# Kernel optimization log

Measured on AMD Instinct MI355X. Metric: run time of the kernel, lower is better.

The kernel has to match this reference:

```python
import jax, jax.numpy as jnp
import numpy as np

HIDDEN = 2048
N_HEADS = 16
HEAD_DIM = HIDDEN // N_HEADS
INV_NORM = 1.0 / float(np.sqrt(HEAD_DIM))
BETA = 1.0


def setup_inputs() -> dict:
    key = jax.random.key(0)
    ks = jax.random.split(key, 12)
    B, S, H = 2, 2048, HIDDEN
    scale = 1.0 / float(np.sqrt(H))
    return {
        "hidden_states": jax.random.normal(ks[0], (B, S, H), jnp.float32),
        "residual": jax.random.normal(ks[1], (B, S, H), jnp.float32),
        "alibi": jax.random.normal(ks[2], (B * N_HEADS, 1, S), jnp.float32),
        "Wq": jax.random.normal(ks[3], (H, H), jnp.float32) * scale,
        "bq": jnp.zeros((H,), jnp.float32),
        "Wk": jax.random.normal(ks[4], (H, H), jnp.float32) * scale,
        "bk": jnp.zeros((H,), jnp.float32),
        "Wv": jax.random.normal(ks[5], (H, H), jnp.float32) * scale,
        "bv": jnp.zeros((H,), jnp.float32),
        "Wd": jax.random.normal(ks[6], (H, H), jnp.float32) * scale,
        "bd": jnp.zeros((H,), jnp.float32),
    }


def reference(hidden_states, residual, alibi, Wq, bq, Wk, bk, Wv, bv, Wd, bd):
    B, S, H = hidden_states.shape
    # separate QKV projections (nn.Linear: x @ W^T + b)
    q = hidden_states @ Wq.T + bq
    k = hidden_states @ Wk.T + bk
    v = hidden_states @ Wv.T + bv
    # [B, n_heads, S, head_dim]
    q = q.reshape(B, S, N_HEADS, HEAD_DIM).transpose(0, 2, 1, 3)
    k = k.reshape(B, S, N_HEADS, HEAD_DIM).transpose(0, 2, 1, 3)
    v = v.reshape(B, S, N_HEADS, HEAD_DIM).transpose(0, 2, 1, 3)
    # baddbmm: scores = beta * alibi + inv_norm * q @ k^T, per (batch*head)
    alibi_bh = alibi.reshape(B, N_HEADS, 1, S)  # broadcasts over query dim
    scores = BETA * alibi_bh + INV_NORM * jnp.einsum("bhqd,bhkd->bhqk", q, k)
    probs = jax.nn.softmax(scores.astype(jnp.float32), axis=-1).astype(v.dtype)
    # attention dropout: p=0.0 (identity)
    ctx = jnp.einsum("bhqk,bhkd->bhqd", probs, v)  # [B,H,S,D]
    ctx = ctx.transpose(0, 2, 1, 3).reshape(B, S, H)
    out = ctx @ Wd.T + bd
    # hidden dropout p=0.0 then residual add (dropout_add)
    return out + residual
```

## Files before the change

kernel.cpp:

```cpp
#include <hip/hip_runtime.h>

#define HID   2048
#define NHEAD 16
#define HD    128
#define SEQ   2048
#define BATCH 2
#define MROWS (BATCH*SEQ)
#define NQKV  (3*HID)
#define INV_NORM 0.08838834764831845f
#define LOG2E    1.4426950408889634f
#define SCALE_L2 (INV_NORM*LOG2E)

typedef __attribute__((ext_vector_type(8)))  __bf16 bf16x8;
typedef __attribute__((ext_vector_type(4)))  float  f32x4;
typedef __attribute__((ext_vector_type(16))) float  f32x16;

typedef __attribute__((address_space(1))) void GV;
typedef __attribute__((address_space(3))) void LV;

__device__ __forceinline__ void async16(const void* g, void* l) {
  __builtin_amdgcn_global_load_lds((const GV*)g, (LV*)l, 16, 0, 0);
}

__device__ __forceinline__ unsigned short f2bf(float f) {
  unsigned u = __builtin_bit_cast(unsigned, f);
  u += 0x7FFFu + ((u >> 16) & 1u);
  return (unsigned short)(u >> 16);
}

__device__ __forceinline__ unsigned pkbf(float a, float b) {
#if __has_builtin(__builtin_amdgcn_cvt_pk_bf16_f32)
  typedef __attribute__((ext_vector_type(2))) __bf16 bf16x2;
  bf16x2 r = __builtin_amdgcn_cvt_pk_bf16_f32(a, b);
  return __builtin_bit_cast(unsigned, r);
#else
  return (unsigned)f2bf(a) | ((unsigned)f2bf(b) << 16);
#endif
}

__device__ __forceinline__ void pl32swap(unsigned &a, unsigned &b) {
#if __has_builtin(__builtin_amdgcn_permlane32_swap)
  typedef __attribute__((ext_vector_type(2))) unsigned u32x2;
  u32x2 r = __builtin_amdgcn_permlane32_swap(a, b, false, false);
  a = r[0]; b = r[1];
#else
  asm volatile("v_permlane32_swap_b32 %0, %1" : "+v"(a), "+v"(b));
#endif
}

__device__ __forceinline__ void mfma16(f32x4& c, bf16x8 a, bf16x8 b) {
  c = __builtin_amdgcn_mfma_f32_16x16x32_bf16(a, b, c, 0, 0, 0);
}

__device__ __forceinline__ bf16x8 frag(const unsigned short* buf, int row, int chunk) {
  return *(const bf16x8*)(buf + ((row * 8 + (chunk ^ (row & 7))) << 3));
}

__global__ __launch_bounds__(256) void cvt_all_kernel(
    const float* __restrict__ hidden,
    const float* __restrict__ W0, const float* __restrict__ W1,
    const float* __restrict__ W2, const float* __restrict__ W3,
    unsigned short* __restrict__ Xb) {
  const int sel = blockIdx.y;
  const float* src;
  unsigned short* dst;
  int n;
  if (sel == 0) { src = hidden; dst = Xb; n = MROWS * HID; }
  else {
    src = (sel == 1) ? W0 : (sel == 2) ? W1 : (sel == 3) ? W2 : W3;
    dst = Xb + (size_t)MROWS * HID + (size_t)(sel - 1) * HID * HID;
    n = HID * HID;
  }
  int i = (blockIdx.x * 256 + threadIdx.x) * 4;
  if (i >= n) return;
  float4 v = *(const float4*)(src + i);
  ushort4 o;
  o.x = f2bf(v.x); o.y = f2bf(v.y); o.z = f2bf(v.z); o.w = f2bf(v.w);
  *(ushort4*)(dst + i) = o;
}

#define BUFU (24576)
#define BUF3 (3 * BUFU)

__global__ __launch_bounds__(512, 2) void gemm_qkv384_kernel(
    const unsigned short* __restrict__ Xb, const unsigned short* __restrict__ Wb,
    const float* __restrict__ bq, const float* __restrict__ bk,
    const float* __restrict__ bv, unsigned short* __restrict__ Cout) {
  __shared__ __align__(16) unsigned short smem[BUF3];

  const int tid  = threadIdx.x;
  const int w    = tid >> 6;
  const int lane = tid & 63;
  const int l16  = lane & 15;
  const int quad = lane >> 4;
  const int wm   = (w & 3) * 64;
  const int wn   = (w >> 2) * 64;

  const int wg = blockIdx.x;
  const int sw = (wg & 7) * 32 + (wg >> 3);
  const int m0  = (sw & 15) * 256;
  const int rn0 = (sw >> 4) * 384;

  const int sr  = tid >> 3;
  const int scs = ((tid & 7) ^ (sr & 7)) * 8;
  const unsigned short* aBase = Xb + (size_t)(m0 + sr) * HID + scs;

#define STGA(UB, RB, KT)                                              \
  async16(aBase + (size_t)(RB) * HID + (KT),                          \
          (char*)smem + (UB) * 2 + (RB) * 128 + w * 1024)
#define STGB(UB, RB, KT)                                              \
  async16(bBase + (size_t)(RB) * HID + (KT),                          \
          (char*)smem + (UB) * 2 + 32768 + (RB) * 128 + w * 1024)

#define VM6  asm volatile("s_waitcnt vmcnt(6)" ::: "memory")
#define VM0  asm volatile("s_waitcnt vmcnt(0)" ::: "memory")

#define PHASE(UB, KK, STGBLK, WAITBLK)                                         \
  {                                                                            \
    const unsigned short* Ab = smem + (UB);                                    \
    const unsigned short* Bb = Ab + 16384;                                     \
    bf16x8 ta[4], tb[4];                                                       \
    ta[0] = frag(Ab, wm + l16, (KK) * 4 + quad);                               \
    _Pragma("unroll")                                                          \
    for (int j = 0; j < 4; ++j)  tb[j] = frag(Bb, wn + j * 16 + l16, (KK) * 4 + quad); \
    _Pragma("unroll")                                                          \
    for (int ii = 1; ii < 4; ++ii) ta[ii] = frag(Ab, wm + ii * 16 + l16, (KK) * 4 + quad); \
    STGBLK;                                                                    \
    __builtin_amdgcn_s_setprio(1);                                             \
    _Pragma("unroll")                                                          \
    for (int ii = 0; ii < 4; ++ii)                                             \
      _Pragma("unroll")                                                        \
      for (int j = 0; j < 4; ++j) mfma16(acc[ii][j], ta[ii], tb[j]);           \
    __builtin_amdgcn_s_setprio(0);                                             \
    asm volatile("s_waitcnt lgkmcnt(0)" ::: "memory");                         \
    WAITBLK;                                                                   \
    __builtin_amdgcn_s_barrier();                                              \
  }

  for (int p = 0; p < 3; ++p) {
    const unsigned short* bBase = Wb + (size_t)(rn0 + p * 128 + sr) * HID + scs;

    f32x4 acc[4][4];
    const f32x4 zero = {0.f, 0.f, 0.f, 0.f};
#pragma unroll
    for (int a = 0; a < 4; ++a)
#pragma unroll
      for (int j = 0; j < 4; ++j) acc[a][j] = zero;

    STGA(0, 0, 0);  STGA(0, 64, 0);  STGA(0, 128, 0);  STGA(0, 192, 0);
    STGB(0, 0, 0);  STGB(0, 64, 0);
    STGA(BUFU, 0, 64);  STGA(BUFU, 64, 64);  STGA(BUFU, 128, 64);  STGA(BUFU, 192, 64);
    STGB(BUFU, 0, 64);  STGB(BUFU, 64, 64);
    VM6;
    __builtin_amdgcn_s_barrier();

    int kb = 0;
    for (int g = 0; g < 5; ++g) {
      PHASE(0,        0, { STGA(2*BUFU, 0, kb+128); STGA(2*BUFU, 64, kb+128); STGA(2*BUFU, 128, kb+128); }, {});
      PHASE(0,        1, { STGA(2*BUFU, 192, kb+128); STGB(2*BUFU, 0, kb+128); STGB(2*BUFU, 64, kb+128); }, VM6);
      PHASE(BUFU,     0, { STGA(0, 0, kb+192); STGA(0, 64, kb+192); STGA(0, 128, kb+192); }, {});
      PHASE(BUFU,     1, { STGA(0, 192, kb+192); STGB(0, 0, kb+192); STGB(0, 64, kb+192); }, VM6);
      PHASE(2*BUFU,   0, { STGA(BUFU, 0, kb+256); STGA(BUFU, 64, kb+256); STGA(BUFU, 128, kb+256); }, {});
      PHASE(2*BUFU,   1, { STGA(BUFU, 192, kb+256); STGB(BUFU, 0, kb+256); STGB(BUFU, 64, kb+256); }, VM6);
      PHASE(0,        0, { STGA(2*BUFU, 0, kb+320); STGA(2*BUFU, 64, kb+320); STGA(2*BUFU, 128, kb+320); }, {});
      PHASE(0,        1, { STGA(2*BUFU, 192, kb+320); STGB(2*BUFU, 0, kb+320); STGB(2*BUFU, 64, kb+320); }, VM6);
      PHASE(BUFU,     0, { STGA(0, 0, kb+384); STGA(0, 64, kb+384); STGA(0, 128, kb+384); }, {});
      PHASE(BUFU,     1, { STGA(0, 192, kb+384); STGB(0, 0, kb+384); STGB(0, 64, kb+384); }, VM6);
      PHASE(2*BUFU,   0, { STGA(BUFU, 0, kb+448); STGA(BUFU, 64, kb+448); STGA(BUFU, 128, kb+448); }, {});
      PHASE(2*BUFU,   1, { STGA(BUFU, 192, kb+448); STGB(BUFU, 0, kb+448); STGB(BUFU, 64, kb+448); }, VM6);
      kb += 384;
    }

    PHASE(0,    0, {}, {});
    PHASE(0,    1, {}, VM0);
    PHASE(BUFU, 0, {}, {});
    PHASE(BUFU, 1, {}, {});

#pragma unroll
    for (int j = 0; j < 4; ++j) {
      int ng = rn0 + p * 128 + wn + j * 16 + l16;
      float bias = (ng < HID) ? bq[ng] : (ng < 2 * HID ? bk[ng - HID] : bv[ng - 2 * HID]);
#pragma unroll
      for (int a = 0; a < 4; ++a)
#pragma unroll
        for (int r = 0; r < 4; ++r) {
          int mg = m0 + wm + a * 16 + quad * 4 + r;
          Cout[(size_t)mg * NQKV + ng] = f2bf(acc[a][j][r] + bias);
        }
    }
  }
#undef STGA
#undef STGB
#undef PHASE
#undef VM6
#undef VM0
}

__global__ __launch_bounds__(512, 2) void gemm_out384_kernel(
    const unsigned short* __restrict__ Ctx, const unsigned short* __restrict__ Wdb,
    const float* __restrict__ bd, const float* __restrict__ Res,
    float* __restrict__ Out) {
  __shared__ __align__(16) unsigned short smem[BUF3];

  const int tid  = threadIdx.x;
  const int w    = tid >> 6;
  const int lane = tid & 63;
  const int l16  = lane & 15;
  const int quad = lane >> 4;
  const int wm   = (w & 3) * 64;
  const int wn   = (w >> 2) * 64;

  const int wg = blockIdx.x;
  const int sw = (wg & 7) * 32 + (wg >> 3);
  const int m0  = (sw & 15) * 256;
  const int rn0 = (sw >> 4) * 128;

  const int sr  = tid >> 3;
  const int scs = ((tid & 7) ^ (sr & 7)) * 8;
  const unsigned short* aBase = Ctx + (size_t)(m0 + sr) * HID + scs;
  const unsigned short* bBase = Wdb + (size_t)(rn0 + sr) * HID + scs;

#define STGA(UB, RB, KT)                                              \
  async16(aBase + (size_t)(RB) * HID + (KT),                          \
          (char*)smem + (UB) * 2 + (RB) * 128 + w * 1024)
#define STGB(UB, RB, KT)                                              \
  async16(bBase + (size_t)(RB) * HID + (KT),                          \
          (char*)smem + (UB) * 2 + 32768 + (RB) * 128 + w * 1024)

#define VM6  asm volatile("s_waitcnt vmcnt(6)" ::: "memory")
#define VM0  asm volatile("s_waitcnt vmcnt(0)" ::: "memory")

#define PHASE(UB, KK, STGBLK, WAITBLK)                                         \
  {                                                                            \
    const unsigned short* Ab = smem + (UB);                                    \
    const unsigned short* Bb = Ab + 16384;                                     \
    bf16x8 ta[4], tb[4];                                                       \
    ta[0] = frag(Ab, wm + l16, (KK) * 4 + quad);                               \
    _Pragma("unroll")                                                          \
    for (int j = 0; j < 4; ++j)  tb[j] = frag(Bb, wn + j * 16 + l16, (KK) * 4 + quad); \
    _Pragma("unroll")                                                          \
    for (int ii = 1; ii < 4; ++ii) ta[ii] = frag(Ab, wm + ii * 16 + l16, (KK) * 4 + quad); \
    STGBLK;                                                                    \
    __builtin_amdgcn_s_setprio(1);                                             \
    _Pragma("unroll")                                                          \
    for (int ii = 0; ii < 4; ++ii)                                             \
      _Pragma("unroll")                                                        \
      for (int j = 0; j < 4; ++j) mfma16(acc[ii][j], ta[ii], tb[j]);           \
    __builtin_amdgcn_s_setprio(0);                                             \
    asm volatile("s_waitcnt lgkmcnt(0)" ::: "memory");                         \
    WAITBLK;                                                                   \
    __builtin_amdgcn_s_barrier();                                              \
  }

  f32x4 acc[4][4];
  const f32x4 zero = {0.f, 0.f, 0.f, 0.f};
#pragma unroll
  for (int a = 0; a < 4; ++a)
#pragma unroll
    for (int j = 0; j < 4; ++j) acc[a][j] = zero;

  STGA(0, 0, 0);  STGA(0, 64, 0);  STGA(0, 128, 0);  STGA(0, 192, 0);
  STGB(0, 0, 0);  STGB(0, 64, 0);
  STGA(BUFU, 0, 64);  STGA(BUFU, 64, 64);  STGA(BUFU, 128, 64);  STGA(BUFU, 192, 64);
  STGB(BUFU, 0, 64);  STGB(BUFU, 64, 64);
  VM6;
  __builtin_amdgcn_s_barrier();

  int kb = 0;
  for (int g = 0; g < 5; ++g) {
    PHASE(0,        0, { STGA(2*BUFU, 0, kb+128); STGA(2*BUFU, 64, kb+128); STGA(2*BUFU, 128, kb+128); }, {});
    PHASE(0,        1, { STGA(2*BUFU, 192, kb+128); STGB(2*BUFU, 0, kb+128); STGB(2*BUFU, 64, kb+128); }, VM6);
    PHASE(BUFU,     0, { STGA(0, 0, kb+192); STGA(0, 64, kb+192); STGA(0, 128, kb+192); }, {});
    PHASE(BUFU,     1, { STGA(0, 192, kb+192); STGB(0, 0, kb+192); STGB(0, 64, kb+192); }, VM6);
    PHASE(2*BUFU,   0, { STGA(BUFU, 0, kb+256); STGA(BUFU, 64, kb+256); STGA(BUFU, 128, kb+256); }, {});
    PHASE(2*BUFU,   1, { STGA(BUFU, 192, kb+256); STGB(BUFU, 0, kb+256); STGB(BUFU, 64, kb+256); }, VM6);
    PHASE(0,        0, { STGA(2*BUFU, 0, kb+320); STGA(2*BUFU, 64, kb+320); STGA(2*BUFU, 128, kb+320); }, {});
    PHASE(0,        1, { STGA(2*BUFU, 192, kb+320); STGB(2*BUFU, 0, kb+320); STGB(2*BUFU, 64, kb+320); }, VM6);
    PHASE(BUFU,     0, { STGA(0, 0, kb+384); STGA(0, 64, kb+384); STGA(0, 128, kb+384); }, {});
    PHASE(BUFU,     1, { STGA(0, 192, kb+384); STGB(0, 0, kb+384); STGB(0, 64, kb+384); }, VM6);
    PHASE(2*BUFU,   0, { STGA(BUFU, 0, kb+448); STGA(BUFU, 64, kb+448); STGA(BUFU, 128, kb+448); }, {});
    PHASE(2*BUFU,   1, { STGA(BUFU, 192, kb+448); STGB(BUFU, 0, kb+448); STGB(BUFU, 64, kb+448); }, VM6);
    kb += 384;
  }

  PHASE(0,    0, {}, {});
  PHASE(0,    1, {}, VM0);
  PHASE(BUFU, 0, {}, {});
  PHASE(BUFU, 1, {}, {});

#pragma unroll
  for (int j = 0; j < 4; ++j) {
    int ng = rn0 + wn + j * 16 + l16;
    float bias = bd[ng];
#pragma unroll
    for (int a = 0; a < 4; ++a)
#pragma unroll
      for (int r = 0; r < 4; ++r) {
        int mg = m0 + wm + a * 16 + quad * 4 + r;
        size_t off = (size_t)mg * HID + ng;
        Out[off] = acc[a][j][r] + bias + Res[off];
      }
  }
#undef STGA
#undef STGB
#undef PHASE
#undef VM6
#undef VM0
}

__global__ __launch_bounds__(256) void vtrans_kernel(const unsigned short* __restrict__ QKV,
                                                     unsigned short* __restrict__ Vt) {
  __shared__ __align__(16) unsigned short T[64][72];
  const int s0 = blockIdx.x * 64, d0 = blockIdx.y * 64, bh = blockIdx.z;
  const int b = bh >> 4, h = bh & 15;
  const int tid = threadIdx.x;
#pragma unroll
  for (int i = 0; i < 2; ++i) {
    int idx = i * 256 + tid;
    int r = idx >> 3, ch = idx & 7;
    const unsigned short* g = QKV + ((size_t)b * SEQ + s0 + r) * NQKV + 2 * HID + h * HD + d0 + ch * 8;
    *(uint4*)(&T[r][ch * 8]) = *(const uint4*)g;
  }
  __syncthreads();
#pragma unroll
  for (int i = 0; i < 2; ++i) {
    int idx = i * 256 + tid;
    int d = idx >> 3, ch = idx & 7;
    unsigned short v[8];
#pragma unroll
    for (int x = 0; x < 8; ++x) v[x] = T[ch * 8 + x][d];
    unsigned short* g = Vt + ((size_t)bh * HD + d0 + d) * SEQ + s0 + ch * 8;
    *(uint4*)g = *(const uint4*)v;
  }
}

__global__ __launch_bounds__(256, 2) void attn_kernel(
    const unsigned short* __restrict__ QKV, const unsigned short* __restrict__ Vt,
    const float* __restrict__ alibi, unsigned short* __restrict__ Ctx) {
  __shared__ __align__(16) char smem[73728];
  unsigned short* Ks0  = (unsigned short*)smem;
  unsigned short* Ks1  = (unsigned short*)(smem + 16384);
  unsigned short* Vts0 = (unsigned short*)(smem + 32768);
  unsigned short* Vts1 = (unsigned short*)(smem + 49152);
  float*          Alsf = (float*)(smem + 65536);
  unsigned short* Qs   = (unsigned short*)smem;

  const int tid = threadIdx.x, w = tid >> 6, lane = tid & 63;
  const int l32 = lane & 31, h = lane >> 5;
  const int bid = blockIdx.x;
  const int t  = bid >> 3;
  const int q0 = (t & 15) * 128;
  const int bh = (bid & 7) + 8 * (t >> 4);
  const int b = bh >> 4, hh = bh & 15;
  const size_t rowbase = (size_t)b * SEQ;
  const float* ali = alibi + (size_t)bh * SEQ;
  const unsigned short* Vbh = Vt + (size_t)bh * HD * SEQ;

  {
    const unsigned short* qbase = QKV + (rowbase + q0) * NQKV + hh * HD;
#pragma unroll
    for (int i = 0; i < 8; ++i) {
      int slot = i * 256 + w * 64 + lane;
      int r = slot >> 4, c = (slot & 15) ^ (r & 15);
      async16(qbase + (size_t)r * NQKV + c * 8, (char*)Qs + (size_t)(i * 256 + w * 64) * 16);
    }
    const char* asrc = (const char*)ali;
#pragma unroll
    for (int i = 0; i < 2; ++i) {
      int slot = i * 256 + w * 64 + lane;
      async16(asrc + (size_t)slot * 16, (char*)Alsf + (size_t)(i * 256 + w * 64) * 16);
    }
  }
  __syncthreads();
  bf16x8 qf[8];
  {
    int qr = w * 32 + l32;
#pragma unroll
    for (int ks = 0; ks < 8; ++ks) {
      int c = (ks * 2 + h) ^ (qr & 15);
      qf[ks] = *(const bf16x8*)(Qs + (qr * 16 + c) * 8);
    }
  }

  f32x16 oacc[4];
  float l_acc = 0.f;
#pragma unroll
  for (int nb = 0; nb < 4; ++nb)
#pragma unroll
    for (int r = 0; r < 16; ++r) oacc[nb][r] = 0.f;

  __syncthreads();

#define STAGE_KV(T, KD, VD)                                                      \
  {                                                                              \
    const unsigned short* kbase = QKV + (rowbase + (T) * 64) * NQKV + HID + hh * HD; \
    _Pragma("unroll")                                                            \
    for (int i = 0; i < 4; ++i) {                                                \
      int slot = i * 256 + w * 64 + lane;                                        \
      int r = slot >> 4, c = (slot & 15) ^ (r & 15);                             \
      async16(kbase + (size_t)r * NQKV + c * 8, (char*)(KD) + (size_t)(i * 256 + w * 64) * 16); \
    }                                                                            \
    const unsigned short* vbase = Vbh + (T) * 64;                                \
    _Pragma("unroll")                                                            \
    for (int i = 0; i < 4; ++i) {                                                \
      int slot = i * 256 + w * 64 + lane;                                        \
      int r = slot >> 3, c = (slot & 7) ^ (r & 7);                               \
      async16(vbase + (size_t)r * SEQ + c * 8, (char*)(VD) + (size_t)(i * 256 + w * 64) * 16); \
    }                                                                            \
  }

  STAGE_KV(0, Ks0, Vts0);
  STAGE_KV(1, Ks1, Vts1);
  asm volatile("s_waitcnt vmcnt(8)" ::: "memory");
  __builtin_amdgcn_s_barrier();

  for (int kt = 0; kt < SEQ / 64; ++kt) {
    const unsigned short* Kc = (kt & 1) ? Ks1 : Ks0;
    const unsigned short* Vc = (kt & 1) ? Vts1 : Vts0;

    f32x16 sacc[2];
#pragma unroll
    for (int mb = 0; mb < 2; ++mb)
#pragma unroll
      for (int r = 0; r < 16; ++r) sacc[mb][r] = 0.f;
    __builtin_amdgcn_s_setprio(1);
#pragma unroll
    for (int ks = 0; ks < 8; ++ks) {
#pragma unroll
      for (int mb = 0; mb < 2; ++mb) {
        bf16x8 kf = *(const bf16x8*)(Kc + ((mb * 32 + l32) * 16 + ((ks * 2 + h) ^ (l32 & 15))) * 8);
        sacc[mb] = __builtin_amdgcn_mfma_f32_32x32x16_bf16(kf, qf[ks], sacc[mb], 0, 0, 0);
      }
    }
    __builtin_amdgcn_s_setprio(0);

    const float* alsk = Alsf + kt * 64 + 4 * h;
    bf16x8 pfr[4];
#pragma unroll
    for (int mb = 0; mb < 2; ++mb) {
      float p[16];
#pragma unroll
      for (int g = 0; g < 4; ++g) {
        float4 av = *(const float4*)(alsk + mb * 32 + g * 8);
        p[g * 4 + 0] = __builtin_amdgcn_exp2f(sacc[mb][g * 4 + 0] * SCALE_L2 + av.x * LOG2E);
        p[g * 4 + 1] = __builtin_amdgcn_exp2f(sacc[mb][g * 4 + 1] * SCALE_L2 + av.y * LOG2E);
        p[g * 4 + 2] = __builtin_amdgcn_exp2f(sacc[mb][g * 4 + 2] * SCALE_L2 + av.z * LOG2E);
        p[g * 4 + 3] = __builtin_amdgcn_exp2f(sacc[mb][g * 4 + 3] * SCALE_L2 + av.w * LOG2E);
        l_acc += (p[g * 4 + 0] + p[g * 4 + 1]) + (p[g * 4 + 2] + p[g * 4 + 3]);
      }
      unsigned c0 = pkbf(p[0],  p[1]),  c1 = pkbf(p[2],  p[3]);
      unsigned c2 = pkbf(p[4],  p[5]),  c3 = pkbf(p[6],  p[7]);
      unsigned c4 = pkbf(p[8],  p[9]),  c5 = pkbf(p[10], p[11]);
      unsigned c6 = pkbf(p[12], p[13]), c7 = pkbf(p[14], p[15]);
      pl32swap(c0, c2);  pl32swap(c1, c3);
      pl32swap(c4, c6);  pl32swap(c5, c7);
      uint4 f0; f0.x = c0; f0.y = c1; f0.z = c2; f0.w = c3;
      uint4 f1; f1.x = c4; f1.y = c5; f1.z = c6; f1.w = c7;
      pfr[mb * 2 + 0] = __builtin_bit_cast(bf16x8, f0);
      pfr[mb * 2 + 1] = __builtin_bit_cast(bf16x8, f1);
    }

    __builtin_amdgcn_s_setprio(1);
#pragma unroll
    for (int ks2 = 0; ks2 < 4; ++ks2) {
      bf16x8 pf = pfr[ks2];
#pragma unroll
      for (int nb = 0; nb < 4; ++nb) {
        bf16x8 vf = *(const bf16x8*)(Vc + ((nb * 32 + l32) * 8 + ((ks2 * 2 + h) ^ (l32 & 7))) * 8);
        oacc[nb] = __builtin_amdgcn_mfma_f32_32x32x16_bf16(pf, vf, oacc[nb], 0, 0, 0);
      }
    }
    __builtin_amdgcn_s_setprio(0);

    asm volatile("s_waitcnt lgkmcnt(0) vmcnt(0)" ::: "memory");
    __builtin_amdgcn_s_barrier();
    if (kt + 2 < SEQ / 64) {
      unsigned short* kd = (kt & 1) ? Ks1 : Ks0;
      unsigned short* vd = (kt & 1) ? Vts1 : Vts0;
      STAGE_KV(kt + 2, kd, vd);
    }
  }
#undef STAGE_KV

  float lf = l_acc + __shfl_xor(l_acc, 32, 64);
  float rinv[16];
#pragma unroll
  for (int reg = 0; reg < 16; ++reg) {
    int row = (reg & 3) + 8 * (reg >> 2) + 4 * h;
    rinv[reg] = 1.0f / __shfl(lf, row, 64);
  }

#pragma unroll
  for (int nb = 0; nb < 4; ++nb)
#pragma unroll
    for (int reg = 0; reg < 16; ++reg) {
      int row = (reg & 3) + 8 * (reg >> 2) + 4 * h;
      size_t qg = rowbase + q0 + w * 32 + row;
      Ctx[qg * HID + hh * HD + nb * 32 + l32] = f2bf(oacc[nb][reg] * rinv[reg]);
    }
}

extern "C" void kernel_launch(void* const* d_in, const int* in_sizes, int n_in,
                              void* d_out, int out_size, void* d_ws, size_t ws_size,
                              hipStream_t stream) {
  const float* hidden   = (const float*)d_in[0];
  const float* residual = (const float*)d_in[1];
  const float* alibi    = (const float*)d_in[2];
  const float* Wq = (const float*)d_in[3];
  const float* bq = (const float*)d_in[4];
  const float* Wk = (const float*)d_in[5];
  const float* bk = (const float*)d_in[6];
  const float* Wv = (const float*)d_in[7];
  const float* bv = (const float*)d_in[8];
  const float* Wd = (const float*)d_in[9];
  const float* bd = (const float*)d_in[10];
  float* out = (float*)d_out;

  unsigned short* Xb    = (unsigned short*)d_ws;
  unsigned short* Wqkvb = Xb + (size_t)MROWS * HID;
  unsigned short* Wdb   = Wqkvb + (size_t)NQKV * HID;
  unsigned short* QKVb  = Wdb + (size_t)HID * HID;
  unsigned short* Ctxb  = QKVb + (size_t)MROWS * NQKV;
  unsigned short* Vtb   = Wqkvb;

  cvt_all_kernel<<<dim3(MROWS * HID / 4 / 256, 5), 256, 0, stream>>>(hidden, Wq, Wk, Wv, Wd, Xb);

  gemm_qkv384_kernel<<<256, 512, 0, stream>>>(Xb, Wqkvb, bq, bk, bv, QKVb);
  vtrans_kernel<<<dim3(SEQ / 64, HD / 64, BATCH * NHEAD), 256, 0, stream>>>(QKVb, Vtb);
  attn_kernel<<<512, 256, 0, stream>>>(QKVb, Vtb, alibi, Ctxb);
  gemm_out384_kernel<<<256, 512, 0, stream>>>(Ctxb, Wdb, bd, residual, out);
}
```

Baseline: 433.9 us.

## Software-pipeline attention QK^T with softmax/PV and flatten conversion grid

The attention loop is restructured into a two-tile software pipeline: the QK^T MFMAs for the next KV tile are issued alongside the softmax and PV of the current tile. K and V staging are split so each buffer is refilled as soon as it is consumed, with finer waitcnt/barrier placement. This is meant to hide exp/softmax latency behind matrix work and to overlap loads better, at the cost of more live accumulator registers and a hardcoded sequence-length schedule. The conversion kernel is also flattened to a 1D grid, which removes the idle blocks that the weight slices launched in the old 2D grid.

```diff
diff --git a/kernel.cpp b/kernel.cpp
--- a/kernel.cpp
+++ b/kernel.cpp
@@ -61,22 +61,20 @@
     const float* __restrict__ W0, const float* __restrict__ W1,
     const float* __restrict__ W2, const float* __restrict__ W3,
     unsigned short* __restrict__ Xb) {
-  const int sel = blockIdx.y;
+  size_t e = ((size_t)blockIdx.x * 256 + threadIdx.x) * 4;
   const float* src;
-  unsigned short* dst;
-  int n;
-  if (sel == 0) { src = hidden; dst = Xb; n = MROWS * HID; }
-  else {
-    src = (sel == 1) ? W0 : (sel == 2) ? W1 : (sel == 3) ? W2 : W3;
-    dst = Xb + (size_t)MROWS * HID + (size_t)(sel - 1) * HID * HID;
-    n = HID * HID;
-  }
-  int i = (blockIdx.x * 256 + threadIdx.x) * 4;
-  if (i >= n) return;
-  float4 v = *(const float4*)(src + i);
+  if (e < (size_t)MROWS * HID) {
+    src = hidden + e;
+  } else {
+    size_t r = e - (size_t)MROWS * HID;
+    int sel = (int)(r >> 22);
+    size_t off = r & ((1u << 22) - 1);
+    src = ((sel == 0) ? W0 : (sel == 1) ? W1 : (sel == 2) ? W2 : W3) + off;
+  }
+  float4 v = *(const float4*)src;
   ushort4 o;
   o.x = f2bf(v.x); o.y = f2bf(v.y); o.z = f2bf(v.z); o.w = f2bf(v.w);
-  *(ushort4*)(dst + i) = o;
+  *(ushort4*)(Xb + e) = o;
 }
 
 #define BUFU (24576)
@@ -391,15 +389,18 @@
 
   __syncthreads();
 
-#define STAGE_KV(T, KD, VD)                                                      \
+#define STAGE_K(T, KD)                                                           \
   {                                                                              \
-    const unsigned short* kbase = QKV + (rowbase + (T) * 64) * NQKV + HID + hh * HD; \
+    const unsigned short* kbase = QKV + (rowbase + (size_t)(T) * 64) * NQKV + HID + hh * HD; \
     _Pragma("unroll")                                                            \
     for (int i = 0; i < 4; ++i) {                                                \
       int slot = i * 256 + w * 64 + lane;                                        \
       int r = slot >> 4, c = (slot & 15) ^ (r & 15);                             \
       async16(kbase + (size_t)r * NQKV + c * 8, (char*)(KD) + (size_t)(i * 256 + w * 64) * 16); \
     }                                                                            \
+  }
+#define STAGE_V(T, VD)                                                           \
+  {                                                                              \
     const unsigned short* vbase = Vbh + (T) * 64;                                \
     _Pragma("unroll")                                                            \
     for (int i = 0; i < 4; ++i) {                                                \
@@ -409,78 +410,106 @@
     }                                                                            \
   }
 
-  STAGE_KV(0, Ks0, Vts0);
-  STAGE_KV(1, Ks1, Vts1);
+#define QKT(SACC, KBUF)                                                          \
+  {                                                                              \
+    _Pragma("unroll")                                                            \
+    for (int mb = 0; mb < 2; ++mb)                                               \
+      _Pragma("unroll")                                                          \
+      for (int r = 0; r < 16; ++r) (SACC)[mb][r] = 0.f;                          \
+    __builtin_amdgcn_s_setprio(1);                                               \
+    _Pragma("unroll")                                                            \
+    for (int ks = 0; ks < 8; ++ks)                                               \
+      _Pragma("unroll")                                                          \
+      for (int mb = 0; mb < 2; ++mb) {                                           \
+        bf16x8 kf = *(const bf16x8*)((KBUF) + ((mb * 32 + l32) * 16 + ((ks * 2 + h) ^ (l32 & 15))) * 8); \
+        (SACC)[mb] = __builtin_amdgcn_mfma_f32_32x32x16_bf16(kf, qf[ks], (SACC)[mb], 0, 0, 0); \
+      }                                                                          \
+    __builtin_amdgcn_s_setprio(0);                                               \
+  }
+
+#define SOFTMAX(SACC, KT, PFR)                                                   \
+  {                                                                              \
+    const float* alsk = Alsf + (KT) * 64 + 4 * h;                                \
+    _Pragma("unroll")                                                            \
+    for (int mb = 0; mb < 2; ++mb) {                                             \
+      float p[16];                                                               \
+      _Pragma("unroll")                                                          \
+      for (int g = 0; g < 4; ++g) {                                              \
+        float4 av = *(const float4*)(alsk + mb * 32 + g * 8);                    \
+        p[g * 4 + 0] = __builtin_amdgcn_exp2f((SACC)[mb][g * 4 + 0] * SCALE_L2 + av.x * LOG2E); \
+        p[g * 4 + 1] = __builtin_amdgcn_exp2f((SACC)[mb][g * 4 + 1] * SCALE_L2 + av.y * LOG2E); \
+        p[g * 4 + 2] = __builtin_amdgcn_exp2f((SACC)[mb][g * 4 + 2] * SCALE_L2 + av.z * LOG2E); \
+        p[g * 4 + 3] = __builtin_amdgcn_exp2f((SACC)[mb][g * 4 + 3] * SCALE_L2 + av.w * LOG2E); \
+        l_acc += (p[g * 4 + 0] + p[g * 4 + 1]) + (p[g * 4 + 2] + p[g * 4 + 3]);  \
+      }                                                                          \
+      unsigned c0 = pkbf(p[0],  p[1]),  c1 = pkbf(p[2],  p[3]);                  \
+      unsigned c2 = pkbf(p[4],  p[5]),  c3 = pkbf(p[6],  p[7]);                  \
+      unsigned c4 = pkbf(p[8],  p[9]),  c5 = pkbf(p[10], p[11]);                 \
+      unsigned c6 = pkbf(p[12], p[13]), c7 = pkbf(p[14], p[15]);                 \
+      pl32swap(c0, c2);  pl32swap(c1, c3);                                       \
+      pl32swap(c4, c6);  pl32swap(c5, c7);                                       \
+      uint4 f0; f0.x = c0; f0.y = c1; f0.z = c2; f0.w = c3;                      \
+      uint4 f1; f1.x = c4; f1.y = c5; f1.z = c6; f1.w = c7;                      \
+      (PFR)[mb * 2 + 0] = __builtin_bit_cast(bf16x8, f0);                        \
+      (PFR)[mb * 2 + 1] = __builtin_bit_cast(bf16x8, f1);                        \
+    }                                                                            \
+  }
+
+#define PVOP(PFR, VBUF)                                                          \
+  {                                                                              \
+    __builtin_amdgcn_s_setprio(1);                                               \
+    _Pragma("unroll")                                                            \
+    for (int ks2 = 0; ks2 < 4; ++ks2) {                                          \
+      bf16x8 pf = (PFR)[ks2];                                                    \
+      _Pragma("unroll")                                                          \
+      for (int nb = 0; nb < 4; ++nb) {                                           \
+        bf16x8 vf = *(const bf16x8*)((VBUF) + ((nb * 32 + l32) * 8 + ((ks2 * 2 + h) ^ (l32 & 7))) * 8); \
+        oacc[nb] = __builtin_amdgcn_mfma_f32_32x32x16_bf16(pf, vf, oacc[nb], 0, 0, 0); \
+      }                                                                          \
+    }                                                                            \
+    __builtin_amdgcn_s_setprio(0);                                               \
+  }
+
+  STAGE_K(0, Ks0);  STAGE_V(0, Vts0);
+  STAGE_K(1, Ks1);  STAGE_V(1, Vts1);
   asm volatile("s_waitcnt vmcnt(8)" ::: "memory");
   __builtin_amdgcn_s_barrier();
 
-  for (int kt = 0; kt < SEQ / 64; ++kt) {
-    const unsigned short* Kc = (kt & 1) ? Ks1 : Ks0;
-    const unsigned short* Vc = (kt & 1) ? Vts1 : Vts0;
-
-    f32x16 sacc[2];
-#pragma unroll
-    for (int mb = 0; mb < 2; ++mb)
-#pragma unroll
-      for (int r = 0; r < 16; ++r) sacc[mb][r] = 0.f;
-    __builtin_amdgcn_s_setprio(1);
-#pragma unroll
-    for (int ks = 0; ks < 8; ++ks) {
-#pragma unroll
-      for (int mb = 0; mb < 2; ++mb) {
-        bf16x8 kf = *(const bf16x8*)(Kc + ((mb * 32 + l32) * 16 + ((ks * 2 + h) ^ (l32 & 15))) * 8);
-        sacc[mb] = __builtin_amdgcn_mfma_f32_32x32x16_bf16(kf, qf[ks], sacc[mb], 0, 0, 0);
-      }
-    }
-    __builtin_amdgcn_s_setprio(0);
-
-    const float* alsk = Alsf + kt * 64 + 4 * h;
-    bf16x8 pfr[4];
-#pragma unroll
-    for (int mb = 0; mb < 2; ++mb) {
-      float p[16];
-#pragma unroll
-      for (int g = 0; g < 4; ++g) {
-        float4 av = *(const float4*)(alsk + mb * 32 + g * 8);
-        p[g * 4 + 0] = __builtin_amdgcn_exp2f(sacc[mb][g * 4 + 0] * SCALE_L2 + av.x * LOG2E);
-        p[g * 4 + 1] = __builtin_amdgcn_exp2f(sacc[mb][g * 4 + 1] * SCALE_L2 + av.y * LOG2E);
-        p[g * 4 + 2] = __builtin_amdgcn_exp2f(sacc[mb][g * 4 + 2] * SCALE_L2 + av.z * LOG2E);
-        p[g * 4 + 3] = __builtin_amdgcn_exp2f(sacc[mb][g * 4 + 3] * SCALE_L2 + av.w * LOG2E);
-        l_acc += (p[g * 4 + 0] + p[g * 4 + 1]) + (p[g * 4 + 2] + p[g * 4 + 3]);
-      }
-      unsigned c0 = pkbf(p[0],  p[1]),  c1 = pkbf(p[2],  p[3]);
-      unsigned c2 = pkbf(p[4],  p[5]),  c3 = pkbf(p[6],  p[7]);
-      unsigned c4 = pkbf(p[8],  p[9]),  c5 = pkbf(p[10], p[11]);
-      unsigned c6 = pkbf(p[12], p[13]), c7 = pkbf(p[14], p[15]);
-      pl32swap(c0, c2);  pl32swap(c1, c3);
-      pl32swap(c4, c6);  pl32swap(c5, c7);
-      uint4 f0; f0.x = c0; f0.y = c1; f0.z = c2; f0.w = c3;
-      uint4 f1; f1.x = c4; f1.y = c5; f1.z = c6; f1.w = c7;
-      pfr[mb * 2 + 0] = __builtin_bit_cast(bf16x8, f0);
-      pfr[mb * 2 + 1] = __builtin_bit_cast(bf16x8, f1);
-    }
-
-    __builtin_amdgcn_s_setprio(1);
-#pragma unroll
-    for (int ks2 = 0; ks2 < 4; ++ks2) {
-      bf16x8 pf = pfr[ks2];
-#pragma unroll
-      for (int nb = 0; nb < 4; ++nb) {
-        bf16x8 vf = *(const bf16x8*)(Vc + ((nb * 32 + l32) * 8 + ((ks2 * 2 + h) ^ (l32 & 7))) * 8);
-        oacc[nb] = __builtin_amdgcn_mfma_f32_32x32x16_bf16(pf, vf, oacc[nb], 0, 0, 0);
-      }
-    }
-    __builtin_amdgcn_s_setprio(0);
-
-    asm volatile("s_waitcnt lgkmcnt(0) vmcnt(0)" ::: "memory");
+  f32x16 sA[2], sB[2];
+  QKT(sA, Ks0);
+  asm volatile("s_waitcnt lgkmcnt(0)" ::: "memory");
+  __builtin_amdgcn_s_barrier();
+
+  for (int kt = 0; kt < 30; kt += 2) {
+    STAGE_K(kt + 2, Ks0);
+    asm volatile("s_waitcnt vmcnt(8)" ::: "memory");
+    QKT(sB, Ks1);
+    { bf16x8 pfr[4]; SOFTMAX(sA, kt, pfr); PVOP(pfr, Vts0); }
+    asm volatile("s_waitcnt lgkmcnt(0)" ::: "memory");
     __builtin_amdgcn_s_barrier();
-    if (kt + 2 < SEQ / 64) {
-      unsigned short* kd = (kt & 1) ? Ks1 : Ks0;
-      unsigned short* vd = (kt & 1) ? Vts1 : Vts0;
-      STAGE_KV(kt + 2, kd, vd);
-    }
-  }
-#undef STAGE_KV
+    STAGE_V(kt + 2, Vts0);
+    STAGE_K(kt + 3, Ks1);
+    asm volatile("s_waitcnt vmcnt(8)" ::: "memory");
+    QKT(sA, Ks0);
+    { bf16x8 pfr[4]; SOFTMAX(sB, kt + 1, pfr); PVOP(pfr, Vts1); }
+    asm volatile("s_waitcnt lgkmcnt(0)" ::: "memory");
+    __builtin_amdgcn_s_barrier();
+    STAGE_V(kt + 3, Vts1);
+  }
+
+  asm volatile("s_waitcnt vmcnt(4)" ::: "memory");
+  QKT(sB, Ks1);
+  { bf16x8 pfr[4]; SOFTMAX(sA, 30, pfr); PVOP(pfr, Vts0); }
+  asm volatile("s_waitcnt lgkmcnt(0) vmcnt(0)" ::: "memory");
+  __builtin_amdgcn_s_barrier();
+  { bf16x8 pfr[4]; SOFTMAX(sB, 31, pfr); PVOP(pfr, Vts1); }
+  asm volatile("s_waitcnt lgkmcnt(0)" ::: "memory");
+
+#undef STAGE_K
+#undef STAGE_V
+#undef QKT
+#undef SOFTMAX
+#undef PVOP
 
   float lf = l_acc + __shfl_xor(l_acc, 32, 64);
   float rinv[16];
@@ -523,7 +552,8 @@
   unsigned short* Ctxb  = QKVb + (size_t)MROWS * NQKV;
   unsigned short* Vtb   = Wqkvb;
 
-  cvt_all_kernel<<<dim3(MROWS * HID / 4 / 256, 5), 256, 0, stream>>>(hidden, Wq, Wk, Wv, Wd, Xb);
+  const int nTot = (MROWS * HID + 4 * HID * HID) / 4 / 256;
+  cvt_all_kernel<<<nTot, 256, 0, stream>>>(hidden, Wq, Wk, Wv, Wd, Xb);
 
   gemm_qkv384_kernel<<<256, 512, 0, stream>>>(Xb, Wqkvb, bq, bk, bv, QKVb);
   vtrans_kernel<<<dim3(SEQ / 64, HD / 64, BATCH * NHEAD), 256, 0, stream>>>(QKVb, Vtb);
```

After: 423.9 us. 1.02x faster.
